# Performance work log

Measured on AMD Instinct MI355X. Metric: run time of the kernel, lower is better.

Reference implementation:

```python
import jax, jax.numpy as jnp
import numpy as np

THRESHOLD = 8.0
BN_EPS = 1e-5


def setup_inputs() -> dict:
    key = jax.random.key(0)
    k1, k2 = jax.random.split(key)
    B, C, H, W = 2, 128, 64, 64
    x = jax.random.normal(k1, (B, C, H, W), dtype=jnp.float32)
    W_fc = jax.random.normal(k2, (C, C), dtype=jnp.float32) * (1.0 / np.sqrt(C))
    b_fc = jnp.zeros((C,), dtype=jnp.float32)
    gamma = jnp.ones((C,), dtype=jnp.float32)
    beta = jnp.zeros((C,), dtype=jnp.float32)
    return {"x": x, "W_fc": W_fc, "b_fc": b_fc, "gamma": gamma, "beta": beta}


def _mean_agg(X, path):
    # X: [B,N,C], path: [B,N,N] (col->row). out = rownorm(path) @ X
    out = jnp.matmul(path, X)
    s = jnp.sum(path, axis=2, keepdims=True)  # [B,N,1]
    norm = jnp.where(s > 0, 1.0 / s, 0.0)     # inf -> 0 as in torch code
    return norm * out


def reference(x, W_fc, b_fc, gamma, beta):
    b, c, h, w = x.shape
    N = h * w
    # [B,N,C] token features
    xf = jnp.transpose(x.reshape(b, c, N), (0, 2, 1))
    # pairwise euclidean distance (cdist, p=2)
    sq = jnp.sum(xf * xf, axis=-1)  # [B,N]
    d2 = sq[:, :, None] + sq[:, None, :] - 2.0 * jnp.einsum('bnc,bmc->bnm', xf, xf)
    dist = jnp.sqrt(jnp.maximum(d2, 0.0))
    Hg = (dist < THRESHOLD).astype(xf.dtype)  # [B,N,N] hypergraph incidence
    # HyperGraphConv: y = fc(x); E = mean(H^T @ y); out = mean(H @ E); res = y + out
    y = jnp.einsum('bnc,dc->bnd', xf, W_fc) + b_fc
    E = _mean_agg(y, jnp.swapaxes(Hg, 1, 2))
    x_out = _mean_agg(E, Hg)
    xe = y + x_out  # [B,N,C]
    # back to [B,C,H,W]
    xo = jnp.transpose(xe, (0, 2, 1)).reshape(b, c, h, w)
    # BatchNorm2d (training mode: batch stats over B,H,W) + SiLU
    mean = jnp.mean(xo, axis=(0, 2, 3), keepdims=True)
    var = jnp.var(xo, axis=(0, 2, 3), keepdims=True)
    xn = (xo - mean) * jax.lax.rsqrt(var + BN_EPS)
    xn = gamma[None, :, None, None] * xn + beta[None, :, None, None]
    return xn * jax.nn.sigmoid(xn)
```

## Files before the change

kernel.cpp:

```cpp
#include <hip/hip_runtime.h>
#include <hip/hip_cooperative_groups.h>

namespace cg = cooperative_groups;

typedef unsigned short ushort_t;
typedef unsigned int   uint32;
typedef unsigned long long u64;
typedef __bf16 bf16_t;
typedef bf16_t bf16x8 __attribute__((ext_vector_type(8)));
typedef float  f32x4  __attribute__((ext_vector_type(4)));

#define N_TOK 4096
#define C_DIM 128
#define NTOT  8192
#define THRESH2 64.0f
#define NBLK 1024

#define XF_OFF  (0u)
#define YF_OFF  (2u<<20)
#define EF_OFF  (6u<<20)
#define XE_OFF  (10u<<20)
#define SQ_OFF  (14u<<20)
#define BN_OFF  ((14u<<20) + 32768u)
#define HB_OFF  (16u<<20)
#define WS_NEED ((size_t)(24u<<20))

__device__ __forceinline__ ushort_t f2b(float f){
    uint32 u = __float_as_uint(f);
    u += 0x7fffu + ((u>>16)&1u);
    return (ushort_t)(u>>16);
}
__device__ __forceinline__ u64 shfl_u64(u64 v, int src){
    uint32 lo = (uint32)v, hi = (uint32)(v>>32);
    lo = __shfl(lo, src); hi = __shfl(hi, src);
    return ((u64)hi<<32)|lo;
}
__device__ __forceinline__ u64 shfl_xor_u64(u64 v, int m){
    uint32 lo = (uint32)v, hi = (uint32)(v>>32);
    lo = __shfl_xor(lo, m); hi = __shfl_xor(hi, m);
    return ((u64)hi<<32)|lo;
}

union SMem {
    struct { ushort_t Xs[64*136]; ushort_t Ws[64*136]; } fc;
    struct { ushort_t Al[64*136]; ushort_t Bl[64*136]; u64 rowW[64]; u64 part[256]; } gr;
    struct { float r1[4][128]; float r2[4][128]; } agg;
    struct { float tile[32][33]; } bn;
};

__global__ __launch_bounds__(256, 4) void k_fused(const float* __restrict__ x,
                                                  const float* __restrict__ W,
                                                  const float* __restrict__ bfc,
                                                  const float* __restrict__ gamma,
                                                  const float* __restrict__ beta,
                                                  ushort_t* __restrict__ Xf,
                                                  float* __restrict__ Yf,
                                                  float* __restrict__ Ef,
                                                  float* __restrict__ Xe,
                                                  float* __restrict__ sq,
                                                  float* __restrict__ bnp,
                                                  u64* __restrict__ Hb,
                                                  float* __restrict__ out){
    __shared__ SMem sm;
    cg::grid_group grid = cg::this_grid();
    int tid = threadIdx.x;
    int bid = blockIdx.x;

    if (bid < 256){
        int t0 = (bid >> 1) * 64;
        int dh = bid & 1;
        int b  = t0 >> 12;
        int n0 = t0 & 4095;
        if (bid == 0){
            #pragma unroll
            for (int k=0;k<8;k++) bnp[tid + 256*k] = 0.f;
        }
        const float* xb = x + (size_t)b * C_DIM * N_TOK + n0;
        #pragma unroll
        for (int k=0;k<8;k++){
            int idx = tid + 256*k;
            int c = idx >> 4, n4 = (idx & 15)*4;
            float4 v = *(const float4*)(xb + (size_t)c*N_TOK + n4);
            sm.fc.Xs[(n4+0)*136 + c] = f2b(v.x);
            sm.fc.Xs[(n4+1)*136 + c] = f2b(v.y);
            sm.fc.Xs[(n4+2)*136 + c] = f2b(v.z);
            sm.fc.Xs[(n4+3)*136 + c] = f2b(v.w);
        }
        const float* Wb = W + (size_t)dh*64*C_DIM;
        #pragma unroll
        for (int k=0;k<8;k++){
            int idx = tid + 256*k;
            int d = idx >> 5, c4 = (idx & 31)*4;
            float4 v = *(const float4*)(Wb + d*C_DIM + c4);
            uint2 u;
            u.x = (uint32)f2b(v.x) | ((uint32)f2b(v.y)<<16);
            u.y = (uint32)f2b(v.z) | ((uint32)f2b(v.w)<<16);
            *(uint2*)(&sm.fc.Ws[d*136 + c4]) = u;
        }
        __syncthreads();
        #pragma unroll
        for (int k=0;k<2;k++){
            int idx = tid + 256*(k + 2*dh);
            int row = idx >> 4, c8 = (idx & 15)*8;
            uint4 o = *(const uint4*)(&sm.fc.Xs[row*136 + c8]);
            *(uint4*)(Xf + (size_t)(t0 + row)*C_DIM + c8) = o;
        }
        if (dh == 0){
            int tok = tid >> 2, p = tid & 3;
            const ushort_t* xr = &sm.fc.Xs[tok*136 + p*32];
            float sacc = 0.f;
            #pragma unroll
            for (int i=0;i<16;i++){
                uint32 u = *(const uint32*)(&xr[i*2]);
                float v0 = __uint_as_float(u<<16);
                float v1 = __uint_as_float(u & 0xffff0000u);
                sacc = fmaf(v0, v0, sacc);
                sacc = fmaf(v1, v1, sacc);
            }
            sacc += __shfl_xor(sacc, 1);
            sacc += __shfl_xor(sacc, 2);
            if (p == 0) sq[t0 + tok] = sacc;
        }
        int wv = tid >> 6, lane = tid & 63;
        int qd = lane >> 4, m = lane & 15;
        f32x4 acc[4] = {{0,0,0,0},{0,0,0,0},{0,0,0,0},{0,0,0,0}};
        #pragma unroll
        for (int kc=0;kc<4;kc++){
            bf16x8 af = *(const bf16x8*)(&sm.fc.Xs[(wv*16 + m)*136 + kc*32 + qd*8]);
            #pragma unroll
            for (int ct=0;ct<4;ct++){
                bf16x8 bfr = *(const bf16x8*)(&sm.fc.Ws[(ct*16+m)*136 + kc*32 + qd*8]);
                acc[ct] = __builtin_amdgcn_mfma_f32_16x16x32_bf16(af, bfr, acc[ct], 0, 0, 0);
            }
        }
        int row = t0 + wv*16 + qd*4;
        #pragma unroll
        for (int ct=0;ct<4;ct++){
            int d = dh*64 + ct*16 + m;
            float bias = bfc[d];
            #pragma unroll
            for (int r=0;r<4;r++)
                Yf[(size_t)(row + r)*C_DIM + d] = acc[ct][r] + bias;
        }
    }
    grid.sync();

    for (int item = bid; item < 4160; item += NBLK){
        __syncthreads();
        int bb = (item >= 2080) ? 1 : 0;
        int L = item - bb*2080;
        int bi = (int)((129.0f - sqrtf(16641.0f - 8.0f*(float)L)) * 0.5f);
        while (bi > 0 && bi*(129-bi)/2 > L) --bi;
        while ((bi+1)*(129-(bi+1))/2 <= L) ++bi;
        int bj = bi + (L - bi*(129-bi)/2);
        int i0 = bi*64, j0 = bj*64;
        const ushort_t* XfA = Xf + (size_t)(bb*N_TOK + i0)*C_DIM;
        const ushort_t* XfB = Xf + (size_t)(bb*N_TOK + j0)*C_DIM;
        #pragma unroll
        for (int k=0;k<4;k++){
            int q = tid + 256*k;
            int row = q >> 4, cp = (q & 15)*8;
            *(uint4*)(&sm.gr.Al[row*136 + cp]) = *(const uint4*)(XfA + row*C_DIM + cp);
            *(uint4*)(&sm.gr.Bl[row*136 + cp]) = *(const uint4*)(XfB + row*C_DIM + cp);
        }
        __syncthreads();
        int wv = tid >> 6, lane = tid & 63;
        int qd = lane >> 4, m = lane & 15;
        f32x4 acc[4] = {{0,0,0,0},{0,0,0,0},{0,0,0,0},{0,0,0,0}};
        #pragma unroll
        for (int kc=0;kc<4;kc++){
            bf16x8 a0 = *(const bf16x8*)(&sm.gr.Al[(wv*16 + m)*136 + kc*32 + qd*8]);
            #pragma unroll
            for (int ct=0;ct<4;ct++){
                bf16x8 bfr = *(const bf16x8*)(&sm.gr.Bl[(ct*16+m)*136 + kc*32 + qd*8]);
                acc[ct] = __builtin_amdgcn_mfma_f32_16x16x32_bf16(a0, bfr, acc[ct], 0, 0, 0);
            }
        }
        float sqj[4];
        #pragma unroll
        for (int ct=0;ct<4;ct++) sqj[ct] = sq[bb*N_TOK + j0 + ct*16 + m];
        int lr = wv*16 + qd*4;
        int ib = i0 + lr;
        float sqi[4];
        #pragma unroll
        for (int r=0;r<4;r++) sqi[r] = sq[bb*N_TOK + ib + r];
        #pragma unroll
        for (int r=0;r<4;r++){
            u64 bits = 0;
            #pragma unroll
            for (int ct=0;ct<4;ct++){
                float d2 = sqi[r] + sqj[ct] - 2.0f*acc[ct][r];
                if (d2 < THRESH2) bits |= (u64)1 << (ct*16 + m);
            }
            bits |= shfl_xor_u64(bits, 1);
            bits |= shfl_xor_u64(bits, 2);
            bits |= shfl_xor_u64(bits, 4);
            bits |= shfl_xor_u64(bits, 8);
            if (m == 0){
                Hb[(size_t)(bb*N_TOK + ib + r)*64 + bj] = bits;
                sm.gr.rowW[lr + r] = bits;
            }
        }
        __syncthreads();
        if (bi != bj){
            int jj = tid & 63, q = tid >> 6;
            u64 p = 0;
            int ibase = q*16;
            #pragma unroll
            for (int ii=0; ii<16; ii++)
                p |= ((sm.gr.rowW[ibase + ii] >> jj) & 1ull) << (ibase + ii);
            sm.gr.part[tid] = p;
            __syncthreads();
            if (tid < 64){
                u64 wt = sm.gr.part[tid] | sm.gr.part[tid+64] | sm.gr.part[tid+128] | sm.gr.part[tid+192];
                Hb[(size_t)(bb*N_TOK + j0 + tid)*64 + bi] = wt;
            }
        }
    }
    grid.sync();

    {
        int wv = tid >> 6, lane = tid & 63;
        u64 myw[2];
        float nrm[2];
        #pragma unroll
        for (int k=0;k<2;k++){
            int row = (bid + k*NBLK)*4 + wv;
            u64 w = Hb[(size_t)row*64 + lane];
            myw[k] = w;
            int cnt = __builtin_popcountll(w);
            cnt += __shfl_xor(cnt, 1);
            cnt += __shfl_xor(cnt, 2);
            cnt += __shfl_xor(cnt, 4);
            cnt += __shfl_xor(cnt, 8);
            cnt += __shfl_xor(cnt, 16);
            cnt += __shfl_xor(cnt, 32);
            nrm[k] = (cnt > 0) ? 1.0f/(float)cnt : 0.0f;
        }
        #pragma unroll
        for (int k=0;k<2;k++){
            int row = (bid + k*NBLK)*4 + wv;
            int b = row >> 12;
            const float* Vb = Yf + (size_t)b*N_TOK*C_DIM;
            float acc0 = 0.f, acc1 = 0.f;
            u64 nz = __ballot(myw[k] != 0);
            while (nz){
                int wdi = __builtin_ctzll(nz);
                nz &= nz - 1;
                u64 mw = shfl_u64(myw[k], wdi);
                while (mw){
                    int j = wdi*64 + __builtin_ctzll(mw);
                    mw &= mw - 1;
                    acc0 += Vb[(size_t)j*C_DIM + lane];
                    acc1 += Vb[(size_t)j*C_DIM + lane + 64];
                }
            }
            size_t o = (size_t)row*C_DIM;
            Ef[o + lane]      = acc0*nrm[k];
            Ef[o + lane + 64] = acc1*nrm[k];
        }
        grid.sync();
        float s1a=0.f, s1b=0.f, s2a=0.f, s2b=0.f;
        #pragma unroll
        for (int k=0;k<2;k++){
            int row = (bid + k*NBLK)*4 + wv;
            int b = row >> 12;
            const float* Vb = Ef + (size_t)b*N_TOK*C_DIM;
            float acc0 = 0.f, acc1 = 0.f;
            u64 nz = __ballot(myw[k] != 0);
            while (nz){
                int wdi = __builtin_ctzll(nz);
                nz &= nz - 1;
                u64 mw = shfl_u64(myw[k], wdi);
                while (mw){
                    int j = wdi*64 + __builtin_ctzll(mw);
                    mw &= mw - 1;
                    acc0 += Vb[(size_t)j*C_DIM + lane];
                    acc1 += Vb[(size_t)j*C_DIM + lane + 64];
                }
            }
            size_t o = (size_t)row*C_DIM;
            float xe0 = Yf[o + lane]      + acc0*nrm[k];
            float xe1 = Yf[o + lane + 64] + acc1*nrm[k];
            Xe[o + lane]      = xe0;
            Xe[o + lane + 64] = xe1;
            s1a += xe0; s2a += xe0*xe0;
            s1b += xe1; s2b += xe1*xe1;
        }
        __syncthreads();
        sm.agg.r1[wv][lane]      = s1a;
        sm.agg.r1[wv][lane + 64] = s1b;
        sm.agg.r2[wv][lane]      = s2a;
        sm.agg.r2[wv][lane + 64] = s2b;
        __syncthreads();
        if (tid < 128){
            float s1 = sm.agg.r1[0][tid]+sm.agg.r1[1][tid]+sm.agg.r1[2][tid]+sm.agg.r1[3][tid];
            float s2 = sm.agg.r2[0][tid]+sm.agg.r2[1][tid]+sm.agg.r2[2][tid]+sm.agg.r2[3][tid];
            int prt = bid & 7;
            atomicAdd(&bnp[prt*256 + tid],       s1);
            atomicAdd(&bnp[prt*256 + 128 + tid], s2);
        }
    }
    grid.sync();

    {
        int it = bid;
        int bx = it & 127, byz = it >> 7;
        int by = byz & 3, bz = byz >> 2;
        int tx = tid & 31, ty = tid >> 5;
        int n0 = bx*32, c0 = by*32, b = bz;
        int c = c0 + tx;
        float s1 = 0.f, s2 = 0.f;
        #pragma unroll
        for (int p=0;p<8;p++){
            s1 += bnp[p*256 + c];
            s2 += bnp[p*256 + 128 + c];
        }
        float inv = 1.0f / (float)NTOT;
        float mean = s1 * inv;
        float var  = s2*inv - mean*mean;
        float scale = gamma[c] * rsqrtf(var + 1e-5f);
        float shift = beta[c] - mean*scale;
        #pragma unroll
        for (int k=0;k<4;k++){
            int nl = ty + 8*k;
            float v = Xe[(size_t)(b*N_TOK + n0 + nl)*C_DIM + c];
            v = scale*v + shift;
            float sg = 1.0f/(1.0f + __expf(-v));
            sm.bn.tile[tx][nl] = v * sg;
        }
        __syncthreads();
        #pragma unroll
        for (int k=0;k<4;k++){
            int cl = ty + 8*k;
            out[(size_t)(b*C_DIM + c0 + cl)*N_TOK + n0 + tx] = sm.bn.tile[cl][tx];
        }
    }
}

__global__ __launch_bounds__(256) void k_fc(const float* __restrict__ x,
                                            const float* __restrict__ W,
                                            const float* __restrict__ bfc,
                                            ushort_t* __restrict__ Xf,
                                            float* __restrict__ Yf,
                                            float* __restrict__ sq,
                                            float* __restrict__ bnp){
    __shared__ ushort_t Xs[64*136];
    __shared__ ushort_t Ws[64*136];
    int tid = threadIdx.x;
    int t0 = blockIdx.x * 64;
    int dh = blockIdx.y;
    int b  = t0 >> 12;
    int n0 = t0 & 4095;
    if (blockIdx.x == 0 && dh == 0){
        #pragma unroll
        for (int k=0;k<8;k++) bnp[tid + 256*k] = 0.f;
    }
    const float* xb = x + (size_t)b * C_DIM * N_TOK + n0;
    #pragma unroll
    for (int k=0;k<8;k++){
        int idx = tid + 256*k;
        int c = idx >> 4, n4 = (idx & 15)*4;
        float4 v = *(const float4*)(xb + (size_t)c*N_TOK + n4);
        Xs[(n4+0)*136 + c] = f2b(v.x);
        Xs[(n4+1)*136 + c] = f2b(v.y);
        Xs[(n4+2)*136 + c] = f2b(v.z);
        Xs[(n4+3)*136 + c] = f2b(v.w);
    }
    const float* Wb = W + (size_t)dh*64*C_DIM;
    #pragma unroll
    for (int k=0;k<8;k++){
        int idx = tid + 256*k;
        int d = idx >> 5, c4 = (idx & 31)*4;
        float4 v = *(const float4*)(Wb + d*C_DIM + c4);
        uint2 u;
        u.x = (uint32)f2b(v.x) | ((uint32)f2b(v.y)<<16);
        u.y = (uint32)f2b(v.z) | ((uint32)f2b(v.w)<<16);
        *(uint2*)(&Ws[d*136 + c4]) = u;
    }
    __syncthreads();
    #pragma unroll
    for (int k=0;k<2;k++){
        int idx = tid + 256*(k + 2*dh);
        int row = idx >> 4, c8 = (idx & 15)*8;
        uint4 o = *(const uint4*)(&Xs[row*136 + c8]);
        *(uint4*)(Xf + (size_t)(t0 + row)*C_DIM + c8) = o;
    }
    if (dh == 0){
        int tok = tid >> 2, p = tid & 3;
        const ushort_t* xr = &Xs[tok*136 + p*32];
        float sacc = 0.f;
        #pragma unroll
        for (int i=0;i<16;i++){
            uint32 u = *(const uint32*)(&xr[i*2]);
            float v0 = __uint_as_float(u<<16);
            float v1 = __uint_as_float(u & 0xffff0000u);
            sacc = fmaf(v0, v0, sacc);
            sacc = fmaf(v1, v1, sacc);
        }
        sacc += __shfl_xor(sacc, 1);
        sacc += __shfl_xor(sacc, 2);
        if (p == 0) sq[t0 + tok] = sacc;
    }
    int wv = tid >> 6, lane = tid & 63;
    int qd = lane >> 4, m = lane & 15;
    f32x4 acc[4] = {{0,0,0,0},{0,0,0,0},{0,0,0,0},{0,0,0,0}};
    #pragma unroll
    for (int kc=0;kc<4;kc++){
        bf16x8 af = *(const bf16x8*)(&Xs[(wv*16 + m)*136 + kc*32 + qd*8]);
        #pragma unroll
        for (int ct=0;ct<4;ct++){
            bf16x8 bfr = *(const bf16x8*)(&Ws[(ct*16+m)*136 + kc*32 + qd*8]);
            acc[ct] = __builtin_amdgcn_mfma_f32_16x16x32_bf16(af, bfr, acc[ct], 0, 0, 0);
        }
    }
    int row = t0 + wv*16 + qd*4;
    #pragma unroll
    for (int ct=0;ct<4;ct++){
        int d = dh*64 + ct*16 + m;
        float bias = bfc[d];
        #pragma unroll
        for (int r=0;r<4;r++)
            Yf[(size_t)(row + r)*C_DIM + d] = acc[ct][r] + bias;
    }
}

__global__ __launch_bounds__(256) void k_gram(const ushort_t* __restrict__ Xf,
                                              const float* __restrict__ sq,
                                              u64* __restrict__ Hb){
    __shared__ ushort_t Al[128*136];
    __shared__ ushort_t Bl[64*136];
    __shared__ u64 rowW[128];
    __shared__ u64 part[256];
    int tid = threadIdx.x;
    int L = blockIdx.x, b = blockIdx.y;
    int bi = (int)((65.0f - sqrtf(4225.0f - 4.0f*(float)L)) * 0.5f);
    while (bi > 0 && bi*(65-bi) > L) --bi;
    while ((bi+1)*(65-(bi+1)) <= L) ++bi;
    int bj = L - bi*(65-bi) + 2*bi;
    int i0 = bi*128, j0 = bj*64;
    const ushort_t* XfA = Xf + (size_t)(b*N_TOK + i0)*C_DIM;
    const ushort_t* XfB = Xf + (size_t)(b*N_TOK + j0)*C_DIM;
    #pragma unroll
    for (int k=0;k<8;k++){
        int q = tid + 256*k;
        int row = q >> 4, cp = (q & 15)*8;
        *(uint4*)(&Al[row*136 + cp]) = *(const uint4*)(XfA + row*C_DIM + cp);
    }
    #pragma unroll
    for (int k=0;k<4;k++){
        int q = tid + 256*k;
        int row = q >> 4, cp = (q & 15)*8;
        *(uint4*)(&Bl[row*136 + cp]) = *(const uint4*)(XfB + row*C_DIM + cp);
    }
    __syncthreads();
    int wv = tid >> 6, lane = tid & 63;
    int qd = lane >> 4, m = lane & 15;
    f32x4 acc[2][4] = {{{0,0,0,0},{0,0,0,0},{0,0,0,0},{0,0,0,0}},
                       {{0,0,0,0},{0,0,0,0},{0,0,0,0},{0,0,0,0}}};
    #pragma unroll
    for (int kc=0;kc<4;kc++){
        bf16x8 a0 = *(const bf16x8*)(&Al[(wv*32 +      m)*136 + kc*32 + qd*8]);
        bf16x8 a1 = *(const bf16x8*)(&Al[(wv*32 + 16 + m)*136 + kc*32 + qd*8]);
        #pragma unroll
        for (int ct=0;ct<4;ct++){
            bf16x8 bfr = *(const bf16x8*)(&Bl[(ct*16+m)*136 + kc*32 + qd*8]);
            acc[0][ct] = __builtin_amdgcn_mfma_f32_16x16x32_bf16(a0, bfr, acc[0][ct], 0, 0, 0);
            acc[1][ct] = __builtin_amdgcn_mfma_f32_16x16x32_bf16(a1, bfr, acc[1][ct], 0, 0, 0);
        }
    }
    float sqj[4];
    #pragma unroll
    for (int ct=0;ct<4;ct++) sqj[ct] = sq[b*N_TOK + j0 + ct*16 + m];
    #pragma unroll
    for (int rt=0;rt<2;rt++){
        int lr = wv*32 + rt*16 + qd*4;
        int ib = i0 + lr;
        float sqi[4];
        #pragma unroll
        for (int r=0;r<4;r++) sqi[r] = sq[b*N_TOK + ib + r];
        #pragma unroll
        for (int r=0;r<4;r++){
            u64 bits = 0;
            #pragma unroll
            for (int ct=0;ct<4;ct++){
                float d2 = sqi[r] + sqj[ct] - 2.0f*acc[rt][ct][r];
                if (d2 < THRESH2) bits |= (u64)1 << (ct*16 + m);
            }
            bits |= shfl_xor_u64(bits, 1);
            bits |= shfl_xor_u64(bits, 2);
            bits |= shfl_xor_u64(bits, 4);
            bits |= shfl_xor_u64(bits, 8);
            if (m == 0){
                Hb[(size_t)(b*N_TOK + ib + r)*64 + bj] = bits;
                rowW[lr + r] = bits;
            }
        }
    }
    __syncthreads();
    {
        int jj = tid & 63, hw = (tid>>6)&1, sub = tid>>7;
        u64 p = 0;
        int ibase = hw*64 + sub*32;
        #pragma unroll 8
        for (int ii=0; ii<32; ii++){
            u64 wrd = rowW[ibase + ii];
            p |= ((wrd >> jj) & 1ull) << (sub*32 + ii);
        }
        part[tid] = p;
    }
    __syncthreads();
    if (tid < 128){
        int jj = tid & 63, hw = tid >> 6;
        u64 wt = part[tid] | part[tid + 128];
        Hb[(size_t)(b*N_TOK + j0 + jj)*64 + 2*bi + hw] = wt;
    }
}

template<int MODE>
__global__ __launch_bounds__(256) void k_aggs(const u64* __restrict__ Hb,
                                              const float* __restrict__ V,
                                              const float* __restrict__ Yf,
                                              float* __restrict__ Out,
                                              float* __restrict__ bnp){
    __shared__ float r1[4][128];
    __shared__ float r2[4][128];
    int tid = threadIdx.x;
    int wv = tid >> 6, lane = tid & 63;
    int row = blockIdx.x * 4 + wv;
    int b = row >> 12;
    u64 myw = Hb[(size_t)row*64 + lane];
    int cnt = __builtin_popcountll(myw);
    cnt += __shfl_xor(cnt, 1);
    cnt += __shfl_xor(cnt, 2);
    cnt += __shfl_xor(cnt, 4);
    cnt += __shfl_xor(cnt, 8);
    cnt += __shfl_xor(cnt, 16);
    cnt += __shfl_xor(cnt, 32);
    float acc0 = 0.f, acc1 = 0.f;
    const float* Vb = V + (size_t)b*N_TOK*C_DIM;
    u64 nz = __ballot(myw != 0);
    while (nz){
        int wdi = __builtin_ctzll(nz);
        nz &= nz - 1;
        u64 mw = shfl_u64(myw, wdi);
        while (mw){
            int j = wdi*64 + __builtin_ctzll(mw);
            mw &= mw - 1;
            acc0 += Vb[(size_t)j*C_DIM + lane];
            acc1 += Vb[(size_t)j*C_DIM + lane + 64];
        }
    }
    float norm = (cnt > 0) ? (1.0f/(float)cnt) : 0.0f;
    size_t o = (size_t)row*C_DIM;
    if (MODE == 0){
        Out[o + lane]      = acc0*norm;
        Out[o + lane + 64] = acc1*norm;
    } else {
        float xe0 = Yf[o + lane]      + acc0*norm;
        float xe1 = Yf[o + lane + 64] + acc1*norm;
        Out[o + lane]      = xe0;
        Out[o + lane + 64] = xe1;
        r1[wv][lane]      = xe0;
        r1[wv][lane + 64] = xe1;
        r2[wv][lane]      = xe0*xe0;
        r2[wv][lane + 64] = xe1*xe1;
        __syncthreads();
        if (tid < 128){
            float s1 = r1[0][tid]+r1[1][tid]+r1[2][tid]+r1[3][tid];
            float s2 = r2[0][tid]+r2[1][tid]+r2[2][tid]+r2[3][tid];
            int prt = blockIdx.x & 7;
            atomicAdd(&bnp[prt*256 + tid],       s1);
            atomicAdd(&bnp[prt*256 + 128 + tid], s2);
        }
    }
}

__global__ __launch_bounds__(256) void k_out(const float* __restrict__ Xe,
                                             const float* __restrict__ bnp,
                                             const float* __restrict__ gamma,
                                             const float* __restrict__ beta,
                                             float* __restrict__ out){
    __shared__ float tile[32][33];
    int tx = threadIdx.x, ty = threadIdx.y;
    int n0 = blockIdx.x*32, c0 = blockIdx.y*32, b = blockIdx.z;
    int c = c0 + tx;
    float s1 = 0.f, s2 = 0.f;
    #pragma unroll
    for (int p=0;p<8;p++){
        s1 += bnp[p*256 + c];
        s2 += bnp[p*256 + 128 + c];
    }
    float inv = 1.0f / (float)NTOT;
    float mean = s1 * inv;
    float var  = s2*inv - mean*mean;
    float scale = gamma[c] * rsqrtf(var + 1e-5f);
    float shift = beta[c] - mean*scale;
    #pragma unroll
    for (int k=0;k<4;k++){
        int nl = ty + 8*k;
        float v = Xe[(size_t)(b*N_TOK + n0 + nl)*C_DIM + c];
        v = scale*v + shift;
        float sg = 1.0f/(1.0f + __expf(-v));
        tile[tx][nl] = v * sg;
    }
    __syncthreads();
    #pragma unroll
    for (int k=0;k<4;k++){
        int cl = ty + 8*k;
        out[(size_t)(b*C_DIM + c0 + cl)*N_TOK + n0 + tx] = tile[cl][tx];
    }
}

extern "C" void kernel_launch(void* const* d_in, const int* in_sizes, int n_in,
                              void* d_out, int out_size, void* d_ws, size_t ws_size,
                              hipStream_t stream){
    if (ws_size < WS_NEED) return;
    const float* x     = (const float*)d_in[0];
    const float* W     = (const float*)d_in[1];
    const float* bfc   = (const float*)d_in[2];
    const float* gamma = (const float*)d_in[3];
    const float* beta  = (const float*)d_in[4];
    char* ws = (char*)d_ws;
    ushort_t* Xf = (ushort_t*)(ws + XF_OFF);
    float*    Yf = (float*)(ws + YF_OFF);
    float*    Ef = (float*)(ws + EF_OFF);
    float*    Xe = (float*)(ws + XE_OFF);
    float*    sqp= (float*)(ws + SQ_OFF);
    float*    bnp= (float*)(ws + BN_OFF);
    u64*      Hb = (u64*)(ws + HB_OFF);
    float*    outp = (float*)d_out;

    static int coop_ok = -1;
    if (coop_ok < 0){
        int ok = 0, dev = 0, nb = 0;
        if (hipGetDevice(&dev) == hipSuccess){
            hipDeviceProp_t prop;
            if (hipGetDeviceProperties(&prop, dev) == hipSuccess &&
                hipOccupancyMaxActiveBlocksPerMultiprocessor(&nb, (const void*)k_fused, 256, 0) == hipSuccess){
                ok = (prop.cooperativeLaunch != 0) && (nb * prop.multiProcessorCount >= NBLK);
            }
        }
        coop_ok = ok;
    }

    if (coop_ok){
        void* args[] = {(void*)&x, (void*)&W, (void*)&bfc, (void*)&gamma, (void*)&beta,
                        (void*)&Xf, (void*)&Yf, (void*)&Ef, (void*)&Xe, (void*)&sqp,
                        (void*)&bnp, (void*)&Hb, (void*)&outp};
        hipError_t e = hipLaunchCooperativeKernel((const void*)k_fused, dim3(NBLK), dim3(256),
                                                  args, 0, stream);
        if (e == hipSuccess) return;
    }

    k_fc<<<dim3(128,2), dim3(256), 0, stream>>>(x, W, bfc, Xf, Yf, sqp, bnp);
    k_gram<<<dim3(1056,2), dim3(256), 0, stream>>>(Xf, sqp, Hb);
    k_aggs<0><<<dim3(2048), dim3(256), 0, stream>>>(Hb, Yf, Yf, Ef, bnp);
    k_aggs<1><<<dim3(2048), dim3(256), 0, stream>>>(Hb, Ef, Yf, Xe, bnp);
    k_out<<<dim3(128,4,2), dim3(32,8), 0, stream>>>(Xe, bnp, gamma, beta, outp);
}
```

Before: 112.5 us.

## Fuse two-hop hypergraph aggregation to remove the intermediate edge buffer and grid sync

The two sequential neighbour-aggregation passes, which were split by a grid-wide sync and an Ef buffer in global memory, become one nested pass. For each neighbour j of a row, the kernel reloads j's incidence word, recomputes its degree normalisation and sums Y over j's neighbours inline. This removes one grid.sync and the Ef write and read-back. In exchange, work per row grows with the sum of its neighbours' degrees instead of its own degree, so a dense graph would do much more redundant work than the old two passes.

```diff
diff --git a/kernel.cpp b/kernel.cpp
--- a/kernel.cpp
+++ b/kernel.cpp
@@ -39,6 +39,16 @@
     uint32 lo = (uint32)v, hi = (uint32)(v>>32);
     lo = __shfl_xor(lo, m); hi = __shfl_xor(hi, m);
     return ((u64)hi<<32)|lo;
+}
+__device__ __forceinline__ int wave_popc_reduce(u64 w){
+    int cnt = __builtin_popcountll(w);
+    cnt += __shfl_xor(cnt, 1);
+    cnt += __shfl_xor(cnt, 2);
+    cnt += __shfl_xor(cnt, 4);
+    cnt += __shfl_xor(cnt, 8);
+    cnt += __shfl_xor(cnt, 16);
+    cnt += __shfl_xor(cnt, 32);
+    return cnt;
 }
 
 union SMem {
@@ -221,67 +231,53 @@
 
     {
         int wv = tid >> 6, lane = tid & 63;
-        u64 myw[2];
-        float nrm[2];
-        #pragma unroll
-        for (int k=0;k<2;k++){
-            int row = (bid + k*NBLK)*4 + wv;
-            u64 w = Hb[(size_t)row*64 + lane];
-            myw[k] = w;
-            int cnt = __builtin_popcountll(w);
-            cnt += __shfl_xor(cnt, 1);
-            cnt += __shfl_xor(cnt, 2);
-            cnt += __shfl_xor(cnt, 4);
-            cnt += __shfl_xor(cnt, 8);
-            cnt += __shfl_xor(cnt, 16);
-            cnt += __shfl_xor(cnt, 32);
-            nrm[k] = (cnt > 0) ? 1.0f/(float)cnt : 0.0f;
-        }
+        float s1a=0.f, s1b=0.f, s2a=0.f, s2b=0.f;
         #pragma unroll
         for (int k=0;k<2;k++){
             int row = (bid + k*NBLK)*4 + wv;
             int b = row >> 12;
             const float* Vb = Yf + (size_t)b*N_TOK*C_DIM;
+            u64 myw = Hb[(size_t)row*64 + lane];
+            int cnt = wave_popc_reduce(myw);
+            float nrm_i = (cnt > 0) ? 1.0f/(float)cnt : 0.0f;
             float acc0 = 0.f, acc1 = 0.f;
-            u64 nz = __ballot(myw[k] != 0);
+            u64 nz = __ballot(myw != 0);
             while (nz){
                 int wdi = __builtin_ctzll(nz);
                 nz &= nz - 1;
-                u64 mw = shfl_u64(myw[k], wdi);
+                u64 mw = shfl_u64(myw, wdi);
                 while (mw){
                     int j = wdi*64 + __builtin_ctzll(mw);
                     mw &= mw - 1;
-                    acc0 += Vb[(size_t)j*C_DIM + lane];
-                    acc1 += Vb[(size_t)j*C_DIM + lane + 64];
+                    int jrow = (b << 12) + j;
+                    u64 jw; float nrm_j;
+                    if (jrow == row){
+                        jw = myw; nrm_j = nrm_i;
+                    } else {
+                        jw = Hb[(size_t)jrow*64 + lane];
+                        int jc = wave_popc_reduce(jw);
+                        nrm_j = (jc > 0) ? 1.0f/(float)jc : 0.0f;
+                    }
+                    float sub0 = 0.f, sub1 = 0.f;
+                    u64 jnz = __ballot(jw != 0);
+                    while (jnz){
+                        int w2 = __builtin_ctzll(jnz);
+                        jnz &= jnz - 1;
+                        u64 m2 = shfl_u64(jw, w2);
+                        while (m2){
+                            int kk = w2*64 + __builtin_ctzll(m2);
+                            m2 &= m2 - 1;
+                            sub0 += Vb[(size_t)kk*C_DIM + lane];
+                            sub1 += Vb[(size_t)kk*C_DIM + lane + 64];
+                        }
+                    }
+                    acc0 += nrm_j * sub0;
+                    acc1 += nrm_j * sub1;
                 }
             }
             size_t o = (size_t)row*C_DIM;
-            Ef[o + lane]      = acc0*nrm[k];
-            Ef[o + lane + 64] = acc1*nrm[k];
-        }
-        grid.sync();
-        float s1a=0.f, s1b=0.f, s2a=0.f, s2b=0.f;
-        #pragma unroll
-        for (int k=0;k<2;k++){
-            int row = (bid + k*NBLK)*4 + wv;
-            int b = row >> 12;
-            const float* Vb = Ef + (size_t)b*N_TOK*C_DIM;
-            float acc0 = 0.f, acc1 = 0.f;
-            u64 nz = __ballot(myw[k] != 0);
-            while (nz){
-                int wdi = __builtin_ctzll(nz);
-                nz &= nz - 1;
-                u64 mw = shfl_u64(myw[k], wdi);
-                while (mw){
-                    int j = wdi*64 + __builtin_ctzll(mw);
-                    mw &= mw - 1;
-                    acc0 += Vb[(size_t)j*C_DIM + lane];
-                    acc1 += Vb[(size_t)j*C_DIM + lane + 64];
-                }
-            }
-            size_t o = (size_t)row*C_DIM;
-            float xe0 = Yf[o + lane]      + acc0*nrm[k];
-            float xe1 = Yf[o + lane + 64] + acc1*nrm[k];
+            float xe0 = Yf[o + lane]      + nrm_i*acc0;
+            float xe1 = Yf[o + lane + 64] + nrm_i*acc1;
             Xe[o + lane]      = xe0;
             Xe[o + lane + 64] = xe1;
             s1a += xe0; s2a += xe0*xe0;
```

Result: no change. 112.7 us (+0.2%).
